# Kernel tuning notes

Hardware: AMD Instinct MI355X
Metric: run time of the kernel (lower is better)

## Reference

```python
import jax, jax.numpy as jnp
import numpy as np

D_MODEL = 1024
N_HEADS = 16
HEAD_DIM = D_MODEL // N_HEADS


def setup_inputs() -> dict:
    key = jax.random.key(0)
    k1, k2, k3 = jax.random.split(key, 3)
    B, T = 4, 2048
    x = jax.random.normal(k1, (B, T, D_MODEL), dtype=jnp.float32)
    # torch Linear(d, 3d) weight is [3d, d]; y = x @ W^T. Store as [d, 3d] for x @ W.
    w_qkv = jax.random.normal(k2, (D_MODEL, 3 * D_MODEL), dtype=jnp.float32) * (D_MODEL ** -0.5)
    w_out = jax.random.normal(k3, (D_MODEL, D_MODEL), dtype=jnp.float32) * (D_MODEL ** -0.5)
    return {"x": x, "w_qkv": w_qkv, "w_out": w_out}


def reference(x, w_qkv, w_out):
    B, T, C = x.shape
    qkv = x @ w_qkv                             # [B, T, 3C]
    q, k, v = jnp.split(qkv, 3, axis=2)
    # [B, T, H, Dh] -> work in bthd layout via einsum
    q = q.reshape(B, T, N_HEADS, HEAD_DIM)
    k = k.reshape(B, T, N_HEADS, HEAD_DIM)
    v = v.reshape(B, T, N_HEADS, HEAD_DIM)
    scale = 1.0 / jnp.sqrt(jnp.asarray(HEAD_DIM, dtype=x.dtype))
    attn = jnp.einsum('bqhd,bkhd->bhqk', q, k) * scale   # [B, H, T, T]
    causal = jnp.tril(jnp.ones((T, T), dtype=bool))
    attn = jnp.where(causal, attn, jnp.asarray(-jnp.inf, dtype=attn.dtype))
    attn = jax.nn.softmax(attn, axis=-1)
    out = jnp.einsum('bhqk,bkhd->bqhd', attn, v).reshape(B, T, C)
    return out @ w_out
```

## Files before the change

kernel.cpp:

```cpp
#include <hip/hip_runtime.h>
#include <hip/hip_bf16.h>
#include <cstdint>


typedef __bf16 bf16x8 __attribute__((ext_vector_type(8)));
typedef __bf16 bf16x4 __attribute__((ext_vector_type(4)));
typedef float  f32x4  __attribute__((ext_vector_type(4)));
typedef float  f32x16 __attribute__((ext_vector_type(16)));
typedef unsigned int u32x4 __attribute__((ext_vector_type(4)));
typedef unsigned int u32x2 __attribute__((ext_vector_type(2)));

#define MFMA16(a, b, c) __builtin_amdgcn_mfma_f32_16x16x32_bf16((a), (b), (c), 0, 0, 0)
#define MFMA32(a, b, c) __builtin_amdgcn_mfma_f32_32x32x16_bf16((a), (b), (c), 0, 0, 0)

__device__ __forceinline__ float fexp2(float x) { return __builtin_amdgcn_exp2f(x); }

__device__ __forceinline__ void gload16(const void* g, void* lds) {
  __builtin_amdgcn_global_load_lds(
      (const __attribute__((address_space(1))) void*)(uintptr_t)g,
      (__attribute__((address_space(3))) void*)(uint32_t)(uintptr_t)lds,
      16, 0, 0);
}

__device__ __forceinline__ uint32_t cvtpk(float a, float b) {
  uint32_t r;
  asm("v_cvt_pk_bf16_f32 %0, %1, %2" : "=v"(r) : "v"(a), "v"(b));
  return r;
}

__device__ __forceinline__ float halfswap(float x, int hi) {
  uint32_t u = __builtin_bit_cast(uint32_t, x);
  u32x2 rr = __builtin_amdgcn_permlane32_swap(u, u, false, false);
  return __builtin_bit_cast(float, hi ? rr.x : rr.y);
}

__global__ __launch_bounds__(256) void k_f32_to_bf16(const float* __restrict__ in,
                                                     __bf16* __restrict__ out, int n) {
  int idx = (blockIdx.x * 256 + threadIdx.x) * 4;
  int stride = gridDim.x * 256 * 4;
  for (; idx < n; idx += stride) {
    float4 v = *(const float4*)(in + idx);
    bf16x4 o = { (__bf16)v.x, (__bf16)v.y, (__bf16)v.z, (__bf16)v.w };
    *(bf16x4*)(out + idx) = o;
  }
}

__global__ __launch_bounds__(256) void k_transpose_f32_bf16(const float* __restrict__ in,
                                                            __bf16* __restrict__ out,
                                                            int R, int C, float scale, int nscale) {
  __shared__ float t[64][65];
  const int r0 = blockIdx.y * 64, c0 = blockIdx.x * 64;
  const int tx = threadIdx.x & 15, ty = threadIdx.x >> 4;
#pragma unroll
  for (int rr = 0; rr < 4; ++rr) {
    int r = ty + rr * 16;
    float4 v = *(const float4*)(in + (size_t)(r0 + r) * C + c0 + tx * 4);
    t[r][tx * 4 + 0] = v.x; t[r][tx * 4 + 1] = v.y;
    t[r][tx * 4 + 2] = v.z; t[r][tx * 4 + 3] = v.w;
  }
  __syncthreads();
#pragma unroll
  for (int rr = 0; rr < 4; ++rr) {
    int c = ty + rr * 16;
    float sc = (c0 + c < nscale) ? scale : 1.0f;
    bf16x4 o = { (__bf16)(t[tx * 4 + 0][c] * sc), (__bf16)(t[tx * 4 + 1][c] * sc),
                 (__bf16)(t[tx * 4 + 2][c] * sc), (__bf16)(t[tx * 4 + 3][c] * sc) };
    *(bf16x4*)(out + (size_t)(c0 + c) * R + r0 + tx * 4) = o;
  }
}

template <typename OutT>
__global__ __launch_bounds__(512, 2) void k_gemm128(const __bf16* __restrict__ A,
                                                    const __bf16* __restrict__ BT,
                                                    OutT* __restrict__ C,
                                                    __bf16* __restrict__ VT,
                                                    int M, int N, int K) {
  __shared__ __align__(16) __bf16 SMEM[6][128 * 64];
  const int tid = threadIdx.x;
  const int l = tid & 63, w = tid >> 6;
  const int wm = w >> 2, wn = w & 3;
  const int wnh = wn >> 1, wnl = wn & 1;
  const int lr = l & 15, lk = l >> 4, lr7 = lr & 7;

  const int lin = blockIdx.y * gridDim.x + blockIdx.x;
  const int cpx = (gridDim.x * gridDim.y) >> 3;
  const int swz = (lin & 7) * cpx + (lin >> 3);
  const int bm0 = (swz / gridDim.x) * 128;
  const int bn0 = (swz % gridDim.x) * 256;

  const int sr0 = w * 8 + (l >> 3);
  const int sc0 = ((l & 7) ^ (l >> 3)) * 8;
  const int xo0 = (lk ^ lr7) * 8;
  const int xo1 = ((4 + lk) ^ lr7) * 8;

#define STAGE_A(KT) do {                                                          \
    const __bf16* s_ = A + (size_t)(bm0 + sr0) * K + (KT) * 64 + sc0;             \
    char* d_ = (char*)&SMEM[(KT) & 1][0] + w * 1024;                              \
    gload16(s_, d_);                                                              \
    gload16(s_ + (size_t)64 * K, d_ + 8192);                                      \
  } while (0)
#define STAGE_B(KT, H) do {                                                       \
    const __bf16* s_ = BT + (size_t)(bn0 + (H) * 128 + sr0) * K + (KT) * 64 + sc0; \
    char* d_ = (char*)&SMEM[2 + ((KT) & 1) * 2 + (H)][0] + w * 1024;               \
    gload16(s_, d_);                                                               \
    gload16(s_ + (size_t)64 * K, d_ + 8192);                                       \
  } while (0)
#define LDA(SLOT, QM) do {                                                        \
    _Pragma("unroll") for (int f_ = 0; f_ < 2; ++f_) {                            \
      const __bf16* rp_ = &SMEM[SLOT][0] + (wm * 64 + (QM) * 32 + f_ * 16 + lr) * 64; \
      af[f_][0] = *(const bf16x8*)(rp_ + xo0);                                    \
      af[f_][1] = *(const bf16x8*)(rp_ + xo1);                                    \
    }                                                                             \
  } while (0)
#define LDB(SLOT, QN) do {                                                        \
    _Pragma("unroll") for (int g_ = 0; g_ < 2; ++g_) {                            \
      const __bf16* rp_ = &SMEM[2 + (SLOT) * 2 + wnh][0] +                        \
                          (wnl * 64 + (QN) * 32 + g_ * 16 + lr) * 64;             \
      bq[QN][g_][0] = *(const bf16x8*)(rp_ + xo0);                                \
      bq[QN][g_][1] = *(const bf16x8*)(rp_ + xo1);                                \
    }                                                                             \
  } while (0)
#define MFMAQ(QM, QN) do {                                                        \
    __builtin_amdgcn_s_setprio(1);                                                \
    _Pragma("unroll") for (int f_ = 0; f_ < 2; ++f_) {                            \
      _Pragma("unroll") for (int g_ = 0; g_ < 2; ++g_) {                          \
        acc[(QM) * 2 + f_][(QN) * 2 + g_] =                                       \
            MFMA16(af[f_][0], bq[QN][g_][0], acc[(QM) * 2 + f_][(QN) * 2 + g_]);  \
        acc[(QM) * 2 + f_][(QN) * 2 + g_] =                                       \
            MFMA16(af[f_][1], bq[QN][g_][1], acc[(QM) * 2 + f_][(QN) * 2 + g_]);  \
      }                                                                           \
    }                                                                             \
    __builtin_amdgcn_s_setprio(0);                                                \
  } while (0)
#define BAR() asm volatile("s_barrier" ::: "memory")
#define VMCNT2() asm volatile("s_waitcnt vmcnt(2)" ::: "memory")
#define VMCNT0() asm volatile("s_waitcnt vmcnt(0)" ::: "memory")

  f32x4 acc[4][4];
  const f32x4 fz = {0.f, 0.f, 0.f, 0.f};
#pragma unroll
  for (int m = 0; m < 4; ++m) {
#pragma unroll
    for (int n = 0; n < 4; ++n) acc[m][n] = fz;
  }
  bf16x8 af[2][2], bq[2][2][2];

  STAGE_A(0); STAGE_B(0, 0); STAGE_B(0, 1); STAGE_A(1);
  VMCNT2();
  BAR();

  const int NT = K >> 7;
#pragma unroll 1
  for (int t = 0; t < NT; ++t) {
    const int k1 = 2 * t + 1, k2 = 2 * t + 2, k3 = 2 * t + 3;
    const bool last = (t == NT - 1);
    LDA(0, 0); LDB(0, 0);
    STAGE_B(k1, 0);
    BAR(); MFMAQ(0, 0); BAR();
    LDB(0, 1);
    STAGE_B(k1, 1);
    BAR(); MFMAQ(0, 1); BAR();
    LDA(0, 1);
    BAR(); MFMAQ(1, 1); BAR();
    if (!last) { STAGE_A(k2); VMCNT2(); } else { VMCNT0(); }
    BAR(); MFMAQ(1, 0); BAR();
    LDA(1, 0); LDB(1, 0);
    if (!last) STAGE_B(k2, 0);
    BAR(); MFMAQ(0, 0); BAR();
    LDB(1, 1);
    if (!last) STAGE_B(k2, 1);
    BAR(); MFMAQ(0, 1); BAR();
    LDA(1, 1);
    BAR(); MFMAQ(1, 1); BAR();
    if (!last) { STAGE_A(k3); VMCNT2(); }
    BAR(); MFMAQ(1, 0); BAR();
  }

  if (VT != nullptr && bn0 >= 2048) {
    __bf16* tb = &SMEM[0][0];
    const int LDT = 136;
    const int bb = bm0 >> 11, tbase = bm0 & 2047;
#pragma unroll
    for (int m = 0; m < 4; ++m) {
      const int tt = wm * 64 + m * 16 + lk * 4;
#pragma unroll
      for (int n = 0; n < 4; ++n) {
        const int lcol = wn * 64 + (n >> 1) * 32 + (n & 1) * 16 + lr;
        bf16x4 o = { (__bf16)acc[m][n][0], (__bf16)acc[m][n][1],
                     (__bf16)acc[m][n][2], (__bf16)acc[m][n][3] };
        *(bf16x4*)(tb + lcol * LDT + tt) = o;
      }
    }
    __syncthreads();
#pragma unroll
    for (int it = 0; it < 8; ++it) {
      const int slot = it * 512 + tid;
      const int r = slot >> 4, toff = (slot & 15) * 8;
      bf16x8 v = *(const bf16x8*)(tb + r * LDT + toff);
      const int vcol = (bn0 - 2048) + r;
      const int hc = vcol >> 6, d = vcol & 63;
      *(bf16x8*)(VT + ((size_t)((bb * 16 + hc) * 64 + d)) * 2048 + tbase + toff) = v;
    }
  } else {
#pragma unroll
    for (int m = 0; m < 4; ++m) {
      const int row = bm0 + wm * 64 + m * 16 + lk * 4;
#pragma unroll
      for (int n = 0; n < 4; ++n) {
        const int col = bn0 + wn * 64 + (n >> 1) * 32 + (n & 1) * 16 + lr;
#pragma unroll
        for (int jj = 0; jj < 4; ++jj)
          C[(size_t)(row + jj) * N + col] = (OutT)acc[m][n][jj];
      }
    }
  }
#undef STAGE_A
#undef STAGE_B
#undef LDA
#undef LDB
#undef MFMAQ
#undef BAR
#undef VMCNT2
#undef VMCNT0
}

__global__ __launch_bounds__(256, 2) void k_attn(const __bf16* __restrict__ qkv,
                                                 const __bf16* __restrict__ vt,
                                                 __bf16* __restrict__ ctx) {
  const int id = blockIdx.x;
  const int wg = (id & 7) * 64 + (id >> 3);
  const int p  = wg & 7;
  const int hb = wg >> 3;
  const int h = hb & 15, b = hb >> 4;

  const int l = threadIdx.x & 63, w = threadIdx.x >> 6;
  const int q = l & 31, hi = l >> 5, l7 = l & 7;

  __shared__ __align__(16) __bf16 KVs[3][2][64 * 64];

  const int srow = w * 8 + (l >> 3);
  const int scol = ((l & 7) ^ (l >> 3)) * 8;

  const __bf16* gK0 = qkv + (size_t)(b * 2048 + srow) * 3072 + 1024 + h * 64 + scol;
  const __bf16* gV0 = vt + ((size_t)((b * 16 + h) * 64 + srow)) * 2048 + scol;

  const float NEG = -1e30f;

  bf16x8 ones;
#pragma unroll
  for (int i = 0; i < 8; ++i) ones[i] = (__bf16)1.0f;

#define STG(BUF) do {                                                        \
    char* dK_ = (char*)&KVs[BUF][0][0] + w * 1024;                           \
    char* dV_ = (char*)&KVs[BUF][1][0] + w * 1024;                           \
    gload16(kp, dK_);                                                        \
    gload16(kp + (size_t)32 * 3072, dK_ + 4096);                             \
    gload16(vp, dV_);                                                        \
    gload16(vp + (size_t)32 * 2048, dV_ + 4096);                             \
    kp += (size_t)64 * 3072;                                                 \
    vp += 64;                                                                \
  } while (0)

#define ATTN_TILE(BUF, NXT) do {                                             \
    const int kv0 = kvt * 64;                                                \
    if (kvt + 1 < nkv) {                                                     \
      STG(NXT);                                                              \
      asm volatile("s_waitcnt vmcnt(4)" ::: "memory");                       \
    } else {                                                                 \
      asm volatile("s_waitcnt vmcnt(0)" ::: "memory");                       \
    }                                                                        \
    asm volatile("s_barrier" ::: "memory");                                  \
    if (kvt <= kvlast) {                                                     \
      const __bf16* Kb = &KVs[BUF][0][0];                                    \
      const __bf16* Vb = &KVs[BUF][1][0];                                    \
      f32x16 s0 = (f32x16)(0.0f), s1 = (f32x16)(0.0f);                       \
      __builtin_amdgcn_s_setprio(1);                                         \
      _Pragma("unroll") for (int d0 = 0; d0 < 4; ++d0) {                     \
        bf16x8 k0 = *(const bf16x8*)(Kb + (size_t)q * 64 + (((d0 * 2 + hi) ^ l7) * 8)); \
        bf16x8 k1 = *(const bf16x8*)(Kb + (size_t)(32 + q) * 64 + (((d0 * 2 + hi) ^ l7) * 8)); \
        s0 = MFMA32(k0, qf[d0], s0);                                         \
        s1 = MFMA32(k1, qf[d0], s1);                                         \
      }                                                                      \
      __builtin_amdgcn_s_setprio(0);                                         \
      if (kvt == kvlast) {                                                   \
        _Pragma("unroll") for (int r = 0; r < 16; ++r) {                     \
          const int kl = (r & 3) + 8 * (r >> 2) + 4 * hi;                    \
          if (kv0 + kl > qg) s0[r] = NEG;                                    \
          if (kv0 + 32 + kl > qg) s1[r] = NEG;                               \
        }                                                                    \
      }                                                                      \
      float t[8];                                                            \
      _Pragma("unroll") for (int i = 0; i < 8; ++i)                          \
        t[i] = fmaxf(fmaxf(s0[i], s0[i + 8]), fmaxf(s1[i], s1[i + 8]));      \
      _Pragma("unroll") for (int i = 0; i < 4; ++i) t[i] = fmaxf(t[i], t[i + 4]); \
      float mt = fmaxf(fmaxf(t[0], t[1]), fmaxf(t[2], t[3]));                \
      mt = fmaxf(mt, halfswap(mt, hi));                                      \
      if (!__all(mt - m_run <= 8.0f)) {                                      \
        const float al = fexp2(m_run - mt);                                  \
        _Pragma("unroll") for (int r = 0; r < 16; ++r) {                     \
          o0[r] *= al; o1[r] *= al; os[r] *= al;                             \
        }                                                                    \
        m_run = mt;                                                          \
      }                                                                      \
      _Pragma("unroll") for (int r = 0; r < 16; ++r) {                       \
        s0[r] = fexp2(s0[r] - m_run);                                        \
        s1[r] = fexp2(s1[r] - m_run);                                        \
      }                                                                      \
      uint32_t c0[8], c1[8];                                                 \
      _Pragma("unroll") for (int j = 0; j < 8; ++j) {                        \
        c0[j] = cvtpk(s0[2 * j], s0[2 * j + 1]);                             \
        c1[j] = cvtpk(s1[2 * j], s1[2 * j + 1]);                             \
      }                                                                      \
      u32x4 pk[4];                                                           \
      {                                                                      \
        u32x2 r0 = __builtin_amdgcn_permlane32_swap(c0[0], c0[2], false, false); \
        u32x2 r1 = __builtin_amdgcn_permlane32_swap(c0[1], c0[3], false, false); \
        u32x2 r2 = __builtin_amdgcn_permlane32_swap(c0[4], c0[6], false, false); \
        u32x2 r3 = __builtin_amdgcn_permlane32_swap(c0[5], c0[7], false, false); \
        pk[0].x = r0.x; pk[0].y = r1.x; pk[0].z = r0.y; pk[0].w = r1.y;      \
        pk[1].x = r2.x; pk[1].y = r3.x; pk[1].z = r2.y; pk[1].w = r3.y;      \
        u32x2 r4 = __builtin_amdgcn_permlane32_swap(c1[0], c1[2], false, false); \
        u32x2 r5 = __builtin_amdgcn_permlane32_swap(c1[1], c1[3], false, false); \
        u32x2 r6 = __builtin_amdgcn_permlane32_swap(c1[4], c1[6], false, false); \
        u32x2 r7 = __builtin_amdgcn_permlane32_swap(c1[5], c1[7], false, false); \
        pk[2].x = r4.x; pk[2].y = r5.x; pk[2].z = r4.y; pk[2].w = r5.y;      \
        pk[3].x = r6.x; pk[3].y = r7.x; pk[3].z = r6.y; pk[3].w = r7.y;      \
      }                                                                      \
      bf16x8 pf[4];                                                          \
      _Pragma("unroll") for (int kc = 0; kc < 4; ++kc)                       \
        pf[kc] = __builtin_bit_cast(bf16x8, pk[kc]);                         \
      __builtin_amdgcn_s_setprio(1);                                         \
      _Pragma("unroll") for (int kc = 0; kc < 4; ++kc) {                     \
        bf16x8 vf0 = *(const bf16x8*)(Vb + (size_t)q * 64 + (((kc * 2 + hi) ^ l7) * 8)); \
        o0 = MFMA32(vf0, pf[kc], o0);                                        \
      }                                                                      \
      _Pragma("unroll") for (int kc = 0; kc < 4; ++kc) {                     \
        bf16x8 vf1 = *(const bf16x8*)(Vb + (size_t)(32 + q) * 64 + (((kc * 2 + hi) ^ l7) * 8)); \
        o1 = MFMA32(vf1, pf[kc], o1);                                        \
      }                                                                      \
      _Pragma("unroll") for (int kc = 0; kc < 4; ++kc)                       \
        os = MFMA32(ones, pf[kc], os);         \
      __builtin_amdgcn_s_setprio(0);                                         \
    }                                                                        \
  } while (0)

#pragma unroll 1
  for (int ti = 0; ti < 2; ++ti) {
    const int qb = ti ? p : 15 - p;
    const int q0w = qb * 128 + w * 32;
    const int qg = q0w + q;
    const int nkv = 2 * qb + 2;
    const int kvlast = (q0w + 31) >> 6;

    const __bf16* qp = qkv + (size_t)(b * 2048 + qg) * 3072 + h * 64 + hi * 8;
    bf16x8 qf[4];
#pragma unroll
    for (int d0 = 0; d0 < 4; ++d0) qf[d0] = *(const bf16x8*)(qp + d0 * 16);

    float m_run = NEG;
    f32x16 o0 = (f32x16)(0.0f), o1 = (f32x16)(0.0f), os = (f32x16)(0.0f);

    const __bf16* kp = gK0;
    const __bf16* vp = gV0;

    STG(0);
    int kvt = 0;
    while (true) {
      ATTN_TILE(0, 1); if (++kvt == nkv) break;
      ATTN_TILE(1, 2); if (++kvt == nkv) break;
      ATTN_TILE(2, 0); if (++kvt == nkv) break;
    }
    __syncthreads();

    const float inv = 1.0f / os[0];
    __bf16* Ol = &KVs[0][0][0];
#pragma unroll
    for (int r = 0; r < 16; ++r) {
      const int d = (r & 3) + 8 * (r >> 2) + 4 * hi;
      Ol[(w * 32 + q) * 72 + d]      = (__bf16)(o0[r] * inv);
      Ol[(w * 32 + q) * 72 + 32 + d] = (__bf16)(o1[r] * inv);
    }
    __syncthreads();
    {
      const int row = threadIdx.x >> 1, half = threadIdx.x & 1;
      const __bf16* src = Ol + row * 72 + half * 32;
      __bf16* dst = ctx + (size_t)(b * 2048 + qb * 128 + row) * 1024 + h * 64 + half * 32;
#pragma unroll
      for (int i = 0; i < 4; ++i)
        *(bf16x8*)(dst + i * 8) = *(const bf16x8*)(src + i * 8);
    }
    __syncthreads();
  }
#undef STG
#undef ATTN_TILE
}

extern "C" void kernel_launch(void* const* d_in, const int* in_sizes, int n_in,
                              void* d_out, int out_size, void* d_ws, size_t ws_size,
                              hipStream_t stream) {
  const float* x    = (const float*)d_in[0];
  const float* wqkv = (const float*)d_in[1];
  const float* wout = (const float*)d_in[2];
  float* out = (float*)d_out;

  char* ws = (char*)d_ws;
  __bf16* xb    = (__bf16*)(ws);
  __bf16* wqkvT = (__bf16*)(ws + 16777216);
  __bf16* woutT = (__bf16*)(ws + 23068672);
  __bf16* qkvb  = (__bf16*)(ws + 25165824);
  __bf16* vtb   = (__bf16*)(ws + 75497472);
  __bf16* ctx   = (__bf16*)(ws + 92274688);

  const float qscale = 0.125f * 1.44269504088896340736f;

  k_f32_to_bf16<<<2048, 256, 0, stream>>>(x, xb, 8192 * 1024);
  k_transpose_f32_bf16<<<dim3(48, 16), 256, 0, stream>>>(wqkv, wqkvT, 1024, 3072, qscale, 1024);
  k_transpose_f32_bf16<<<dim3(16, 16), 256, 0, stream>>>(wout, woutT, 1024, 1024, 1.0f, 0);
  k_gemm128<__bf16><<<dim3(12, 64), 512, 0, stream>>>(xb, wqkvT, qkvb, vtb, 8192, 3072, 1024);
  k_attn<<<512, 256, 0, stream>>>(qkvb, vtb, ctx);
  k_gemm128<float><<<dim3(4, 64), 512, 0, stream>>>(ctx, woutT, out, nullptr, 8192, 1024, 1024);
}
```

Measured before the change: 157.7 us.

## Fuse prep kernels into one launch and drop redundant GEMM loop barriers

Merges the x conversion and two weight transpose kernels into a single k_prep launch dispatched by block index, removing two kernel launches and their gaps. In the GEMM main loop, most paired barriers around each MFMA quadrant are removed, leaving barriers only near the A-stage global-to-LDS waits. This aims to cut workgroup synchronization stalls and let LDS reads overlap MFMA work, at the risk of LDS read/write hazards if buffer reuse is not fully covered by the remaining barriers.

```diff
diff --git a/kernel.cpp b/kernel.cpp
--- a/kernel.cpp
+++ b/kernel.cpp
@@ -34,22 +34,33 @@
   return __builtin_bit_cast(float, hi ? rr.x : rr.y);
 }
 
-__global__ __launch_bounds__(256) void k_f32_to_bf16(const float* __restrict__ in,
-                                                     __bf16* __restrict__ out, int n) {
-  int idx = (blockIdx.x * 256 + threadIdx.x) * 4;
-  int stride = gridDim.x * 256 * 4;
-  for (; idx < n; idx += stride) {
-    float4 v = *(const float4*)(in + idx);
-    bf16x4 o = { (__bf16)v.x, (__bf16)v.y, (__bf16)v.z, (__bf16)v.w };
-    *(bf16x4*)(out + idx) = o;
-  }
-}
-
-__global__ __launch_bounds__(256) void k_transpose_f32_bf16(const float* __restrict__ in,
-                                                            __bf16* __restrict__ out,
-                                                            int R, int C, float scale, int nscale) {
+__global__ __launch_bounds__(256) void k_prep(const float* __restrict__ x, __bf16* __restrict__ xb,
+                                              const float* __restrict__ wqkv, __bf16* __restrict__ wqkvT,
+                                              const float* __restrict__ wout, __bf16* __restrict__ woutT,
+                                              float qscale) {
+  const int bid = blockIdx.x;
+  if (bid < 2048) {
+    int idx = (bid * 256 + threadIdx.x) * 4;
+    const int stride = 2048 * 256 * 4;
+    for (; idx < 8192 * 1024; idx += stride) {
+      float4 v = *(const float4*)(x + idx);
+      bf16x4 o = { (__bf16)v.x, (__bf16)v.y, (__bf16)v.z, (__bf16)v.w };
+      *(bf16x4*)(xb + idx) = o;
+    }
+    return;
+  }
+  const float* in; __bf16* out; int R, C, bx, by, nsc; float sc;
+  if (bid < 2816) {
+    const int t2 = bid - 2048;
+    in = wqkv; out = wqkvT; R = 1024; C = 3072; bx = t2 % 48; by = t2 / 48;
+    sc = qscale; nsc = 1024;
+  } else {
+    const int t2 = bid - 2816;
+    in = wout; out = woutT; R = 1024; C = 1024; bx = t2 % 16; by = t2 / 16;
+    sc = 1.0f; nsc = 0;
+  }
   __shared__ float t[64][65];
-  const int r0 = blockIdx.y * 64, c0 = blockIdx.x * 64;
+  const int r0 = by * 64, c0 = bx * 64;
   const int tx = threadIdx.x & 15, ty = threadIdx.x >> 4;
 #pragma unroll
   for (int rr = 0; rr < 4; ++rr) {
@@ -62,9 +73,9 @@
 #pragma unroll
   for (int rr = 0; rr < 4; ++rr) {
     int c = ty + rr * 16;
-    float sc = (c0 + c < nscale) ? scale : 1.0f;
-    bf16x4 o = { (__bf16)(t[tx * 4 + 0][c] * sc), (__bf16)(t[tx * 4 + 1][c] * sc),
-                 (__bf16)(t[tx * 4 + 2][c] * sc), (__bf16)(t[tx * 4 + 3][c] * sc) };
+    float s = (c0 + c < nsc) ? sc : 1.0f;
+    bf16x4 o = { (__bf16)(t[tx * 4 + 0][c] * s), (__bf16)(t[tx * 4 + 1][c] * s),
+                 (__bf16)(t[tx * 4 + 2][c] * s), (__bf16)(t[tx * 4 + 3][c] * s) };
     *(bf16x4*)(out + (size_t)(c0 + c) * R + r0 + tx * 4) = o;
   }
 }
@@ -156,24 +167,28 @@
     const bool last = (t == NT - 1);
     LDA(0, 0); LDB(0, 0);
     STAGE_B(k1, 0);
-    BAR(); MFMAQ(0, 0); BAR();
+    MFMAQ(0, 0);
     LDB(0, 1);
     STAGE_B(k1, 1);
-    BAR(); MFMAQ(0, 1); BAR();
+    MFMAQ(0, 1);
     LDA(0, 1);
-    BAR(); MFMAQ(1, 1); BAR();
+    MFMAQ(1, 1);
+    BAR();
     if (!last) { STAGE_A(k2); VMCNT2(); } else { VMCNT0(); }
-    BAR(); MFMAQ(1, 0); BAR();
+    MFMAQ(1, 0);
+    BAR();
     LDA(1, 0); LDB(1, 0);
     if (!last) STAGE_B(k2, 0);
-    BAR(); MFMAQ(0, 0); BAR();
+    MFMAQ(0, 0);
     LDB(1, 1);
     if (!last) STAGE_B(k2, 1);
-    BAR(); MFMAQ(0, 1); BAR();
+    MFMAQ(0, 1);
     LDA(1, 1);
-    BAR(); MFMAQ(1, 1); BAR();
+    MFMAQ(1, 1);
+    BAR();
     if (!last) { STAGE_A(k3); VMCNT2(); }
-    BAR(); MFMAQ(1, 0); BAR();
+    MFMAQ(1, 0);
+    BAR();
   }
 
   if (VT != nullptr && bn0 >= 2048) {
@@ -413,9 +428,7 @@
 
   const float qscale = 0.125f * 1.44269504088896340736f;
 
-  k_f32_to_bf16<<<2048, 256, 0, stream>>>(x, xb, 8192 * 1024);
-  k_transpose_f32_bf16<<<dim3(48, 16), 256, 0, stream>>>(wqkv, wqkvT, 1024, 3072, qscale, 1024);
-  k_transpose_f32_bf16<<<dim3(16, 16), 256, 0, stream>>>(wout, woutT, 1024, 1024, 1.0f, 0);
+  k_prep<<<3072, 256, 0, stream>>>(x, xb, wqkv, wqkvT, wout, woutT, qscale);
   k_gemm128<__bf16><<<dim3(12, 64), 512, 0, stream>>>(xb, wqkvT, qkvb, vtb, 8192, 3072, 1024);
   k_attn<<<512, 256, 0, stream>>>(qkvb, vtb, ctx);
   k_gemm128<float><<<dim3(4, 64), 512, 0, stream>>>(ctx, woutT, out, nullptr, 8192, 1024, 1024);
```

Result: faster. 149.6 us (-5.1%).
